# Optimization experiments

Measured on AMD Instinct MI355X. Metric: run time of the kernel, lower is better.

Reference implementation:

```python
import jax, jax.numpy as jnp
import numpy as np

B, S, T = 32, 512, 512           # batch, text len, decoder steps
ENC, ATT = 512, 128              # encoder_dim, attention_dim
PH, PO = 256, 256                # prenet hidden/output
DEC, M = 1024, 128               # decoder_rnn_dim, num_mels


def setup_inputs() -> dict:
    key = jax.random.key(0)
    ks = jax.random.split(key, 16)

    def w(k, shape, fan_in):
        return jax.random.normal(k, shape, jnp.float32) / np.float32(np.sqrt(fan_in))

    return {
        "encoder_outputs": jax.random.normal(ks[0], (B, S, ENC), jnp.float32),
        "target_mels": jax.random.normal(ks[1], (B, T, M), jnp.float32),
        # PreNet (dropout in eval mode => identity)
        "pn_w1": w(ks[2], (M, PH), M), "pn_b1": jnp.zeros((PH,), jnp.float32),
        "pn_w2": w(ks[3], (PH, PO), PH), "pn_b2": jnp.zeros((PO,), jnp.float32),
        # AdditiveAttention
        "att_we": w(ks[4], (ENC, ATT), ENC), "att_be": jnp.zeros((ATT,), jnp.float32),
        "att_wd": w(ks[5], (DEC, ATT), DEC), "att_bd": jnp.zeros((ATT,), jnp.float32),
        "att_v": w(ks[6], (ATT,), ATT), "att_vb": jnp.zeros((), jnp.float32),
        # GRU (PyTorch layout: W_ih [3H, in], W_hh [3H, H], gate order r,z,n)
        "gru_wih": w(ks[7], (3 * DEC, PO + ENC), PO + ENC),
        "gru_whh": w(ks[8], (3 * DEC, DEC), DEC),
        "gru_bih": jnp.zeros((3 * DEC,), jnp.float32),
        "gru_bhh": jnp.zeros((3 * DEC,), jnp.float32),
        # output / stop projections
        "out_w": w(ks[9], (DEC + ENC, M), DEC + ENC), "out_b": jnp.zeros((M,), jnp.float32),
        "stop_w": w(ks[10], (DEC + ENC, 1), DEC + ENC), "stop_b": jnp.zeros((1,), jnp.float32),
    }


def reference(encoder_outputs, target_mels, pn_w1, pn_b1, pn_w2, pn_b2,
              att_we, att_be, att_wd, att_bd, att_v, att_vb,
              gru_wih, gru_whh, gru_bih, gru_bhh,
              out_w, out_b, stop_w, stop_b):
    b, t, m = target_mels.shape
    # encoder projection is time-invariant: hoist out of the step loop
    enc_proj = encoder_outputs @ att_we + att_be              # [B,S,A]

    # teacher forcing: prev_mel at step 0 is zeros, then target_mels[:, t-1]
    prev_mels = jnp.concatenate(
        [jnp.zeros((1, b, m), target_mels.dtype),
         jnp.transpose(target_mels, (1, 0, 2))[:-1]], axis=0)  # [T,B,M]

    h0 = jnp.zeros((b, gru_whh.shape[1]), encoder_outputs.dtype)  # [B,DEC]

    def step(h, prev_mel):
        # PreNet (eval mode: dropout = identity)
        x = jax.nn.relu(prev_mel @ pn_w1 + pn_b1)
        x = jax.nn.relu(x @ pn_w2 + pn_b2)                     # [B,PO]
        # additive attention
        dproj = h @ att_wd + att_bd                            # [B,A]
        scores = jnp.tanh(enc_proj + dproj[:, None, :]) @ att_v + att_vb  # [B,S]
        aw = jax.nn.softmax(scores, axis=1)                    # [B,S]
        context = jnp.einsum('bs,bse->be', aw, encoder_outputs)  # [B,ENC]
        # GRU cell (PyTorch gate math, order r,z,n)
        rin = jnp.concatenate([x, context], axis=-1)           # [B,PO+ENC]
        gi = rin @ gru_wih.T + gru_bih                         # [B,3*DEC]
        gh = h @ gru_whh.T + gru_bhh
        ir, iz, inn = jnp.split(gi, 3, axis=-1)
        hr, hz, hn = jnp.split(gh, 3, axis=-1)
        r = jax.nn.sigmoid(ir + hr)
        z = jax.nn.sigmoid(iz + hz)
        n = jnp.tanh(inn + r * hn)
        h_new = (1.0 - z) * n + z * h                          # [B,DEC]
        # projections
        dout = jnp.concatenate([h_new, context], axis=-1)      # [B,DEC+ENC]
        mel = dout @ out_w + out_b                             # [B,M]
        stop = (dout @ stop_w + stop_b)[:, 0]                  # [B]
        return h_new, (mel, stop, aw)

    _, (mels, stops, aws) = jax.lax.scan(step, h0, prev_mels)
    mel_outputs = jnp.transpose(mels, (1, 0, 2))               # [B,T,M]
    stop_tokens = stops.T                                      # [B,T]
    attention_weights = jnp.transpose(aws, (1, 0, 2))          # [B,T,S]
    return (mel_outputs, stop_tokens, attention_weights)
```

## Files before the change

kernel.cpp:

```cpp
#include <hip/hip_runtime.h>

constexpr int B_   = 32;
constexpr int S_   = 512;
constexpr int T_   = 512;
constexpr int ENC_ = 512;
constexpr int ATT_ = 128;
constexpr int PO_  = 256;
constexpr int DEC_ = 1024;
constexpr int M_   = 128;

constexpr int MEL_OFF  = 0;
constexpr int STOP_OFF = B_*T_*M_;
constexpr int AW_OFF   = STOP_OFF + B_*T_;

typedef __attribute__((ext_vector_type(8))) short bf16x8;
typedef __attribute__((ext_vector_type(4))) float f32x4;
typedef unsigned long long ull;

__device__ __forceinline__ float frcp(float x){ return __builtin_amdgcn_rcpf(x); }
__device__ __forceinline__ float ftanh(float x){ float e = __expf(2.f*x); return 1.f - 2.f*frcp(e + 1.f); }
__device__ __forceinline__ float fsig(float x){ return frcp(1.f + __expf(-x)); }

__device__ __forceinline__ float2 upk2(unsigned u){
    return make_float2(__builtin_bit_cast(float, u << 16),
                       __builtin_bit_cast(float, u & 0xffff0000u));
}
__device__ __forceinline__ unsigned short f2b(float f){
    unsigned u = __builtin_bit_cast(unsigned, f);
    return (unsigned short)((u + 0x7fffu + ((u >> 16) & 1u)) >> 16);
}
__device__ __forceinline__ unsigned pk2(float a, float b){
    return (unsigned)f2b(a) | ((unsigned)f2b(b) << 16);
}

__device__ __forceinline__ float ald(const float* p){
    return __hip_atomic_load(p, __ATOMIC_RELAXED, __HIP_MEMORY_SCOPE_AGENT);
}
__device__ __forceinline__ ull ald64(const void* p){
    return __hip_atomic_load((const ull*)p, __ATOMIC_RELAXED, __HIP_MEMORY_SCOPE_AGENT);
}
__device__ __forceinline__ unsigned aldu(const unsigned* p){
    return __hip_atomic_load(p, __ATOMIC_RELAXED, __HIP_MEMORY_SCOPE_AGENT);
}
__device__ __forceinline__ void astf(float* p, float v){
    __hip_atomic_store(p, v, __ATOMIC_RELAXED, __HIP_MEMORY_SCOPE_AGENT);
}
union F2U { float2 f; ull u; };
__device__ __forceinline__ void ast2f(float* p, float a, float b){
    F2U x; x.f = make_float2(a, b);
    __hip_atomic_store((ull*)p, x.u, __ATOMIC_RELAXED, __HIP_MEMORY_SCOPE_AGENT);
}
__device__ __forceinline__ void astu(unsigned* p, unsigned v){
    __hip_atomic_store(p, v, __ATOMIC_RELAXED, __HIP_MEMORY_SCOPE_AGENT);
}

__device__ __forceinline__ void gbarF(unsigned* flags, unsigned ep){
    asm volatile("s_waitcnt vmcnt(0) lgkmcnt(0)" ::: "memory");
    __syncthreads();
    if (threadIdx.x == 0) astu(&flags[blockIdx.x*16], ep);
    if (threadIdx.x < 64){
        for (;;){
            unsigned m = 0xffffffffu;
            #pragma unroll
            for (int q = 0; q < 4; ++q){
                unsigned f = aldu(&flags[(threadIdx.x*4 + q)*16]);
                m = f < m ? f : m;
            }
            if (__all(m >= ep)) break;
            __builtin_amdgcn_s_sleep(1);
        }
    }
    __syncthreads();
}

__device__ __forceinline__ f32x4 mfma16(bf16x8 a, bf16x8 b, f32x4 c){
    return __builtin_amdgcn_mfma_f32_16x16x32_bf16(a, b, c, 0, 0, 0);
}

__global__ __launch_bounds__(256) void k_prep_w(const float* __restrict__ enc,
        const float* __restrict__ whh, const float* __restrict__ wih,
        const float* __restrict__ oww,
        unsigned short* __restrict__ enc_b, unsigned short* __restrict__ wgh,
        unsigned short* __restrict__ wgx, unsigned short* __restrict__ wgc,
        unsigned short* __restrict__ ow_b){
    long long idx = (long long)blockIdx.x*256 + threadIdx.x;
    if (idx < 8388608LL){
        int bh = (int)(idx >> 17); int r = (int)(idx & 131071);
        int s = r >> 9, e = r & 511;
        int b = bh >> 1, half = bh & 1;
        enc_b[idx] = f2b(enc[((size_t)b*S_ + half*256 + s)*ENC_ + e]);
    } else if (idx < 11534336LL){
        long long q = idx - 8388608LL;
        int ds = (int)(q / 98304); int r = (int)(q % 98304);
        int jc = r / 16384; int r2 = r % 16384;
        int kc = r2 >> 9, l = (r2 >> 3) & 63, e = r2 & 7;
        int j = (jc >> 1)*1024 + ds*32 + (jc & 1)*16 + (l & 15);
        int k = kc*32 + ((l >> 4) << 3) + e;
        wgh[q] = f2b(whh[(size_t)j*DEC_ + k]);
    } else if (idx < 12320768LL){
        long long q = idx - 11534336LL;
        int ds = (int)(q / 24576); int r = (int)(q % 24576);
        int jc = r / 4096; int r3 = r % 4096;
        int kc = r3 >> 9, l = (r3 >> 3) & 63, e = r3 & 7;
        int j = (jc >> 1)*1024 + ds*32 + (jc & 1)*16 + (l & 15);
        int k = kc*32 + ((l >> 4) << 3) + e;
        wgx[q] = f2b(wih[(size_t)j*768 + k]);
    } else if (idx < 13893632LL){
        long long q = idx - 12320768LL;
        int ds = (int)(q / 49152); int r = (int)(q % 49152);
        int jc = r / 8192; int r3 = r % 8192;
        int kc = r3 >> 9, l = (r3 >> 3) & 63, e = r3 & 7;
        int j = (jc >> 1)*1024 + ds*32 + (jc & 1)*16 + (l & 15);
        int k = kc*32 + ((l >> 4) << 3) + e;
        wgc[q] = f2b(wih[(size_t)j*768 + 256 + k]);
    } else if (idx < 14090240LL){
        long long q = idx - 13893632LL;
        int cg = (int)(q / 49152); int r = (int)(q % 49152);
        int oc = r / 1536, k = r % 1536;
        ow_b[q] = f2b(oww[(size_t)k*M_ + cg*32 + oc]);
    }
}

__global__ __launch_bounds__(256) void k_encproj(const float* __restrict__ enc,
        const float* __restrict__ we, const float* __restrict__ be,
        unsigned short* __restrict__ ep_b){
    __shared__ float we_s[64*128];
    __shared__ float enc_s[64*64];
    int blk = blockIdx.x, tid = threadIdx.x;
    int b = blk >> 3, ss = blk & 7;
    int s = tid >> 2, ag = tid & 3;
    float acc[32];
    #pragma unroll
    for (int j = 0; j < 32; ++j) acc[j] = 0.f;
    for (int kc = 0; kc < 8; ++kc){
        __syncthreads();
        for (int i = tid; i < 8192; i += 256)
            we_s[i] = we[(size_t)(kc*64 + (i >> 7))*ATT_ + (i & 127)];
        for (int i = tid; i < 4096; i += 256)
            enc_s[i] = enc[((size_t)b*S_ + ss*64 + (i >> 6))*ENC_ + kc*64 + (i & 63)];
        __syncthreads();
        for (int kk = 0; kk < 64; ++kk){
            float ev = enc_s[s*64 + kk];
            const float* wr = &we_s[(kk << 7) + (ag << 5)];
            #pragma unroll
            for (int j = 0; j < 32; ++j) acc[j] += ev*wr[j];
        }
    }
    #pragma unroll
    for (int j = 0; j < 32; ++j){
        int a = (ag << 5) + j;
        ep_b[((size_t)b*512 + ss*64 + s)*ATT_ + a] = f2b(acc[j] + be[a]);
    }
}

__global__ __launch_bounds__(128) void k_prenet(const float* __restrict__ tm,
        const float* __restrict__ w1, const float* __restrict__ b1,
        const float* __restrict__ w2, const float* __restrict__ b2,
        unsigned short* __restrict__ xall){
    __shared__ float mel_l[128*20];
    __shared__ float h1_l[256*20];
    int row0 = blockIdx.x << 4;
    int t = row0 >> 5, b0 = row0 & 31;
    int tid = threadIdx.x;
    for (int p = 0; p < 16; p++){
        int idx = tid + (p << 7);
        int k = idx & 127, r = idx >> 7;
        float v = 0.f;
        if (t > 0) v = tm[((size_t)(b0 + r)*T_ + (t - 1))*M_ + k];
        mel_l[k*20 + r] = v;
    }
    __syncthreads();
    float acc1[16], acc2[16];
    #pragma unroll
    for (int i = 0; i < 16; i++){ acc1[i] = 0.f; acc2[i] = 0.f; }
    for (int k = 0; k < M_; k++){
        float wa = w1[k*256 + tid];
        float wb = w1[k*256 + tid + 128];
        float mv[16];
        *(float4*)&mv[0]  = *(const float4*)&mel_l[k*20 + 0];
        *(float4*)&mv[4]  = *(const float4*)&mel_l[k*20 + 4];
        *(float4*)&mv[8]  = *(const float4*)&mel_l[k*20 + 8];
        *(float4*)&mv[12] = *(const float4*)&mel_l[k*20 + 12];
        #pragma unroll
        for (int r = 0; r < 16; r++){ acc1[r] += mv[r]*wa; acc2[r] += mv[r]*wb; }
    }
    float bb1a = b1[tid], bb1b = b1[tid + 128];
    #pragma unroll
    for (int r = 0; r < 16; r++){
        h1_l[tid*20 + r]         = fmaxf(acc1[r] + bb1a, 0.f);
        h1_l[(tid + 128)*20 + r] = fmaxf(acc2[r] + bb1b, 0.f);
    }
    __syncthreads();
    #pragma unroll
    for (int i = 0; i < 16; i++){ acc1[i] = 0.f; acc2[i] = 0.f; }
    for (int k = 0; k < 256; k++){
        float wa = w2[k*256 + tid];
        float wb = w2[k*256 + tid + 128];
        float mv[16];
        *(float4*)&mv[0]  = *(const float4*)&h1_l[k*20 + 0];
        *(float4*)&mv[4]  = *(const float4*)&h1_l[k*20 + 4];
        *(float4*)&mv[8]  = *(const float4*)&h1_l[k*20 + 8];
        *(float4*)&mv[12] = *(const float4*)&h1_l[k*20 + 12];
        #pragma unroll
        for (int r = 0; r < 16; r++){ acc1[r] += mv[r]*wa; acc2[r] += mv[r]*wb; }
    }
    float bb2a = b2[tid], bb2b = b2[tid + 128];
    #pragma unroll
    for (int r = 0; r < 16; r++){
        xall[((size_t)row0 + r)*PO_ + tid]       = f2b(fmaxf(acc1[r] + bb2a, 0.f));
        xall[((size_t)row0 + r)*PO_ + tid + 128] = f2b(fmaxf(acc2[r] + bb2b, 0.f));
    }
}

#define DYN_BYTES 110592

struct KP {
    const unsigned short* xall_b; const unsigned short* enc_b; const unsigned short* ep_b;
    const unsigned short* wgh; const unsigned short* wgx; const unsigned short* wgc;
    const unsigned short* ow_b;
    const float* awd; const float* sw; const float* bd; const float* av; const float* avb;
    const float* bih; const float* bhh; const float* p_ob; const float* p_sb;
    float* h_f32; unsigned short* h_fb;
    unsigned short* ctx_b; float* den; float* es_b; float* dpp;
    unsigned* flags; float* out;
};

__global__ __launch_bounds__(1024) void k_persist(KP p){
    extern __shared__ char sm[];
    const int bid = blockIdx.x, tid = threadIdx.x;
    const int lane = tid & 63;
    unsigned epn = 0;
    unsigned* flags = p.flags;

    if (bid < 64){
        const int xcd = bid & 7, slot8 = bid >> 3;
        const int ds = xcd*4 + (slot8 >> 1), bh = slot8 & 1;
        unsigned short* hf_b = (unsigned short*)sm;
        char* cf = sm;
        float* pgh_l = (float*)(sm + 32768);
        float* pgx_l = (float*)(sm + 45568);
        float* pgc_l = (float*)(sm + 58368);
        float* h_l   = (float*)(sm + 71168);
        float* rden_l= (float*)(sm + 73216);
        float h_reg = 0.f;

        for (int t = 0; t <= T_; ++t){
            if (t < T_){
                const ull* shb = (const ull*)p.h_fb;
                for (int i = tid; i < 4096; i += 1024){
                    int u = i & 1, l = (i >> 1) & 63, kc = i >> 7;
                    ((ull*)hf_b)[i] = ald64(&shb[(((size_t)bh*32 + kc)*64 + l)*2 + u]);
                }
                __syncthreads();
                int w = tid >> 6;
                if (w < 12){
                    int jc = w >> 1, kg = w & 1;
                    int r4 = lane >> 4, c16 = lane & 15;
                    const bf16x8* Bh = (const bf16x8*)p.wgh +
                        ((size_t)(ds*6 + jc)*32)*64 + lane;
                    f32x4 acc = {0.f,0.f,0.f,0.f};
                    #pragma unroll
                    for (int c = 0; c < 16; ++c){
                        int kc = kg*16 + c;
                        bf16x8 a = *(const bf16x8*)(hf_b + ((kc*64 + lane) << 3));
                        acc = mfma16(a, Bh[kc*64], acc);
                    }
                    #pragma unroll
                    for (int r = 0; r < 4; ++r)
                        pgh_l[(kg*16 + r4*4 + r)*100 + jc*16 + c16] = acc[r];
                    const bf16x8* Xp = (const bf16x8*)p.wgx +
                        ((size_t)(ds*6 + jc)*8)*64 + lane;
                    f32x4 ax = {0.f,0.f,0.f,0.f};
                    #pragma unroll
                    for (int c = 0; c < 4; ++c){
                        int kc = kg*4 + c;
                        bf16x8 a = *(const bf16x8*)(p.xall_b +
                            ((size_t)t*32 + bh*16 + c16)*256 + kc*32 + r4*8);
                        ax = mfma16(a, Xp[kc*64], ax);
                    }
                    #pragma unroll
                    for (int r = 0; r < 4; ++r)
                        pgx_l[(kg*16 + r4*4 + r)*100 + jc*16 + c16] = ax[r];
                }
            }
            gbarF(flags, ++epn);
            if (t < T_){
                const int slot = t & 1;
                if (tid < 16){
                    int b = bh*16 + tid;
                    rden_l[tid] = frcp(ald(&p.den[slot*64 + b]) +
                                       ald(&p.den[slot*64 + 32 + b]));
                }
                __syncthreads();
                {
                    int i = tid;
                    int kc = i >> 6, l = i & 63;
                    int b = bh*16 + (l & 15);
                    int e0 = kc*32 + ((l >> 4) << 3);
                    const ull* c0 = (const ull*)p.ctx_b + (((size_t)slot*2 + 0)*32 + b)*128 + (e0 >> 2);
                    const ull* c1 = (const ull*)p.ctx_b + (((size_t)slot*2 + 1)*32 + b)*128 + (e0 >> 2);
                    ull u00 = ald64(c0), u01 = ald64(c0 + 1);
                    ull u10 = ald64(c1), u11 = ald64(c1 + 1);
                    float rd = rden_l[l & 15];
                    uint2 x0 = __builtin_bit_cast(uint2, u00);
                    uint2 x1 = __builtin_bit_cast(uint2, u01);
                    uint2 y0 = __builtin_bit_cast(uint2, u10);
                    uint2 y1 = __builtin_bit_cast(uint2, u11);
                    float2 a0 = upk2(x0.x), b0 = upk2(y0.x);
                    float2 a1 = upk2(x0.y), b1 = upk2(y0.y);
                    float2 a2 = upk2(x1.x), b2 = upk2(y1.x);
                    float2 a3 = upk2(x1.y), b3 = upk2(y1.y);
                    unsigned w0 = pk2((a0.x + b0.x)*rd, (a0.y + b0.y)*rd);
                    unsigned w1 = pk2((a1.x + b1.x)*rd, (a1.y + b1.y)*rd);
                    unsigned w2 = pk2((a2.x + b2.x)*rd, (a2.y + b2.y)*rd);
                    unsigned w3 = pk2((a3.x + b3.x)*rd, (a3.y + b3.y)*rd);
                    *(uint4*)(cf + (size_t)i*16) = make_uint4(w0, w1, w2, w3);
                }
                __syncthreads();
                int w = tid >> 6;
                if (w < 12){
                    int jc = w >> 1, kg = w & 1;
                    int r4 = lane >> 4, c16 = lane & 15;
                    const bf16x8* Cp = (const bf16x8*)p.wgc +
                        ((size_t)(ds*6 + jc)*16)*64 + lane;
                    f32x4 acc = {0.f,0.f,0.f,0.f};
                    #pragma unroll
                    for (int c = 0; c < 8; ++c){
                        int kc = kg*8 + c;
                        bf16x8 a = *(const bf16x8*)(cf + ((kc*64 + lane) << 4));
                        acc = mfma16(a, Cp[kc*64], acc);
                    }
                    #pragma unroll
                    for (int r = 0; r < 4; ++r)
                        pgc_l[(kg*16 + r4*4 + r)*100 + jc*16 + c16] = acc[r];
                }
                __syncthreads();
                if (tid < 512){
                    int b16 = tid >> 5, dl = tid & 31;
                    int dglob = ds*32 + dl;
                    const float* pa = pgh_l + b16*100;
                    const float* pb = pgh_l + (16 + b16)*100;
                    const float* xa = pgx_l + b16*100;
                    const float* xb = pgx_l + (16 + b16)*100;
                    const float* ca = pgc_l + b16*100;
                    const float* cb = pgc_l + (16 + b16)*100;
                    float gi_r = xa[dl]      + xb[dl]      + ca[dl]      + cb[dl]      + p.bih[dglob];
                    float gi_z = xa[32 + dl] + xb[32 + dl] + ca[32 + dl] + cb[32 + dl] + p.bih[1024 + dglob];
                    float gi_n = xa[64 + dl] + xb[64 + dl] + ca[64 + dl] + cb[64 + dl] + p.bih[2048 + dglob];
                    float gh_r = pa[dl]      + pb[dl]      + p.bhh[dglob];
                    float gh_z = pa[32 + dl] + pb[32 + dl] + p.bhh[1024 + dglob];
                    float gh_n = pa[64 + dl] + pb[64 + dl] + p.bhh[2048 + dglob];
                    float rr = fsig(gi_r + gh_r);
                    float zz = fsig(gi_z + gh_z);
                    float nn = ftanh(gi_n + rr*gh_n);
                    float hv = (1.f - zz)*nn + zz*h_reg;
                    h_reg = hv;
                    h_l[b16*32 + dl] = hv;
                    float hv1 = __shfl_xor(hv, 1);
                    if (!(dl & 1)){
                        int b = bh*16 + b16;
                        ast2f(&p.h_f32[(size_t)((t + 1) & 1)*32768 + (size_t)b*1024 + dglob], hv, hv1);
                        unsigned pkv = pk2(hv, hv1);
                        int l2 = ((dl >> 3) << 4) + b16;
                        size_t fo = (((size_t)bh*32 + ds)*64 + l2)*4 + ((dl & 7) >> 1);
                        astu((unsigned*)p.h_fb + fo, pkv);
                    }
                }
                __syncthreads();
                {
                    int b16 = tid >> 6, ag = tid & 63;
                    int a0 = ag*2;
                    const float* ar = p.awd + (size_t)(ds*32)*128 + a0;
                    float s0 = 0.f, s1 = 0.f;
                    #pragma unroll 8
                    for (int dl = 0; dl < 32; ++dl){
                        float hd = h_l[b16*32 + dl];
                        float2 w2 = *(const float2*)(ar + (size_t)dl*128);
                        s0 += hd*w2.x; s1 += hd*w2.y;
                    }
                    ast2f(&p.dpp[(((size_t)ds*2 + bh)*16 + b16)*128 + a0], s0, s1);
                }
            }
            gbarF(flags, ++epn);
        }
    } else if (bid < 128){
        const int aa = bid - 64, b = aa >> 1, half = aa & 1;
        unsigned short* ep_l = (unsigned short*)sm;
        float* red  = (float*)(sm + 67584);
        float* sred = (float*)(sm + 100992);
        float* dpl  = (float*)(sm + 105088);
        float* avl  = (float*)(sm + 105600);
        float* esl  = (float*)(sm + 106112);
        float* eslt = (float*)(sm + 107136);
        {
            const ull* src = (const ull*)(p.ep_b + ((size_t)b*512 + half*256)*128);
            for (int i = tid; i < 8192; i += 1024){
                int row = i >> 5, col = i & 31;
                ((ull*)ep_l)[(size_t)row*33 + col] = src[i];
            }
            if (tid < 128) avl[tid] = p.av[tid];
        }
        __syncthreads();
        for (int t = 0; t <= T_; ++t){
            if (t < T_){
                const int slot = t & 1;
                {
                    int a = tid & 127, g = tid >> 7;
                    const int bhb = b >> 4, b15 = b & 15;
                    float s = 0.f;
                    #pragma unroll
                    for (int i = 0; i < 4; ++i){
                        int ds2 = g*4 + i;
                        s += ald(&p.dpp[(((size_t)ds2*2 + bhb)*16 + b15)*128 + a]);
                    }
                    red[g*128 + a] = s;
                }
                __syncthreads();
                if (tid < 128){
                    float s = p.bd[tid];
                    #pragma unroll
                    for (int g = 0; g < 8; ++g) s += red[g*128 + tid];
                    dpl[tid] = s;
                }
                __syncthreads();
                {
                    int s = tid >> 2, ao = tid & 3;
                    const ull* er = (const ull*)ep_l + (size_t)s*33 + ao*8;
                    float sc = 0.f;
                    #pragma unroll
                    for (int i = 0; i < 8; ++i){
                        uint2 uu = __builtin_bit_cast(uint2, er[i]);
                        float2 e0 = upk2(uu.x), e1 = upk2(uu.y);
                        int a0 = ao*32 + i*4;
                        sc += ftanh(e0.x + dpl[a0])*avl[a0]
                            + ftanh(e0.y + dpl[a0+1])*avl[a0+1]
                            + ftanh(e1.x + dpl[a0+2])*avl[a0+2]
                            + ftanh(e1.y + dpl[a0+3])*avl[a0+3];
                    }
                    sred[tid] = sc;
                }
                __syncthreads();
                if (tid < 256){
                    float sc = sred[tid*4] + sred[tid*4+1] + sred[tid*4+2] + sred[tid*4+3] + p.avb[0];
                    float ev = __expf(sc);
                    esl[tid] = ev;
                    eslt[(tid & 15)*17 + (tid >> 4)] = ev;
                    astf(&p.es_b[(size_t)slot*16384 + b*512 + half*256 + tid], ev);
                }
                __syncthreads();
                if (tid < 64){
                    float d = esl[tid*4] + esl[tid*4+1] + esl[tid*4+2] + esl[tid*4+3];
                    #pragma unroll
                    for (int m = 1; m <= 32; m <<= 1) d += __shfl_xor(d, m);
                    if (tid == 0) astf(&p.den[slot*64 + half*32 + b], d);
                }
                {
                    int eo = tid >> 4, sg = tid & 15;
                    int e8 = eo*8;
                    const unsigned short* eb = p.enc_b + ((size_t)b*2 + half)*131072;
                    float a0=0,a1=0,a2=0,a3=0,a4=0,a5=0,a6=0,a7=0;
                    #pragma unroll 4
                    for (int i = 0; i < 16; ++i){
                        int s = sg*16 + i;
                        float ev = eslt[i*17 + sg];
                        uint4 u = *(const uint4*)(eb + (size_t)s*512 + e8);
                        float2 v0=upk2(u.x), v1=upk2(u.y), v2=upk2(u.z), v3=upk2(u.w);
                        a0+=ev*v0.x; a1+=ev*v0.y; a2+=ev*v1.x; a3+=ev*v1.y;
                        a4+=ev*v2.x; a5+=ev*v2.y; a6+=ev*v3.x; a7+=ev*v3.y;
                    }
                    float* rr = &red[sg*522 + e8];
                    rr[0]=a0; rr[1]=a1; rr[2]=a2; rr[3]=a3;
                    rr[4]=a4; rr[5]=a5; rr[6]=a6; rr[7]=a7;
                }
                __syncthreads();
                if (tid < 512){
                    float c = 0.f;
                    #pragma unroll
                    for (int sg = 0; sg < 16; ++sg) c += red[sg*522 + tid];
                    float c1 = __shfl_xor(c, 1);
                    if (!(tid & 1))
                        astu((unsigned*)p.ctx_b + (((size_t)slot*2 + half)*32 + b)*256 + (tid >> 1),
                             pk2(c, c1));
                }
            }
            gbarF(flags, ++epn);
            gbarF(flags, ++epn);
        }
    } else {
        const int m = bid - 128, b = m >> 2, q = m & 3;
        unsigned short* ow_l = (unsigned short*)sm;
        float* dout = (float*)(sm + 98432);
        float* redm = (float*)(sm + 104576);
        float* rdm  = (float*)(sm + 108800);
        float* stpr = (float*)(sm + 108816);
        {
            const ull* src = (const ull*)p.ow_b + (size_t)q*12288;
            for (int i = tid; i < 12288; i += 1024){
                int oc = i / 384, kq = i - oc*384;
                uint2 u = __builtin_bit_cast(uint2, src[i]);
                unsigned* d = (unsigned*)ow_l + (size_t)oc*769 + kq*2;
                d[0] = u.x; d[1] = u.y;
            }
        }
        __syncthreads();
        for (int t = 0; t <= T_; ++t){
            gbarF(flags, ++epn);
            if (t >= 1){
                const int slot = (t - 1) & 1;
                if (tid < 512){
                    ull u = ald64((const ull*)p.h_f32 + (size_t)(t & 1)*16384 + (size_t)b*512 + tid);
                    *(float2*)&dout[tid*2] = __builtin_bit_cast(float2, u);
                } else if (tid < 768){
                    int i = tid - 512;
                    unsigned u0 = aldu((const unsigned*)p.ctx_b + (((size_t)slot*2 + 0)*32 + b)*256 + i);
                    unsigned u1 = aldu((const unsigned*)p.ctx_b + (((size_t)slot*2 + 1)*32 + b)*256 + i);
                    float2 f0 = upk2(u0), f1 = upk2(u1);
                    *(float2*)&dout[1024 + i*2] = make_float2(f0.x + f1.x, f0.y + f1.y);
                } else if (tid == 1023){
                    rdm[0] = frcp(ald(&p.den[slot*64 + b]) + ald(&p.den[slot*64 + 32 + b]));
                }
                __syncthreads();
                if (tid < 512) dout[1024 + tid] *= rdm[0];
                __syncthreads();
                {
                    int kg = tid >> 5, oc = tid & 31;
                    const unsigned* wr = (const unsigned*)ow_l + (size_t)oc*769 + kg*24;
                    const float* dr = dout + kg*48;
                    float a = 0.f;
                    #pragma unroll 6
                    for (int i = 0; i < 24; ++i){
                        float2 w2 = upk2(wr[i]);
                        a += dr[i*2]*w2.x + dr[i*2+1]*w2.y;
                    }
                    redm[kg*33 + oc] = a;
                }
                if (q == 0 && tid < 512){
                    int k3 = tid*3;
                    float s = dout[k3]*p.sw[k3] + dout[k3+1]*p.sw[k3+1] + dout[k3+2]*p.sw[k3+2];
                    #pragma unroll
                    for (int mm = 1; mm <= 32; mm <<= 1) s += __shfl_xor(s, mm);
                    if ((tid & 63) == 0) stpr[tid >> 6] = s;
                    float ev = ald(&p.es_b[(size_t)slot*16384 + b*512 + tid]);
                    p.out[AW_OFF + ((size_t)b*T_ + (t-1))*S_ + tid] = ev*rdm[0];
                }
                __syncthreads();
                if (tid < 32){
                    float a = 0.f;
                    #pragma unroll
                    for (int kg = 0; kg < 32; ++kg) a += redm[kg*33 + tid];
                    int c = q*32 + tid;
                    p.out[MEL_OFF + ((size_t)b*T_ + (t-1))*M_ + c] = a + p.p_ob[c];
                } else if (tid == 32 && q == 0){
                    float tot = 0.f;
                    #pragma unroll
                    for (int w2 = 0; w2 < 8; ++w2) tot += stpr[w2];
                    p.out[STOP_OFF + (size_t)b*T_ + (t-1)] = tot + p.p_sb[0];
                }
            }
            gbarF(flags, ++epn);
        }
    }
}

extern "C" void kernel_launch(void* const* d_in, const int* in_sizes, int n_in,
                              void* d_out, int out_size, void* d_ws, size_t ws_size,
                              hipStream_t stream){
    const float* enc = (const float*)d_in[0];
    const float* tm  = (const float*)d_in[1];
    const float* pw1 = (const float*)d_in[2];
    const float* pb1 = (const float*)d_in[3];
    const float* pw2 = (const float*)d_in[4];
    const float* pb2 = (const float*)d_in[5];
    const float* awe = (const float*)d_in[6];
    const float* abe = (const float*)d_in[7];
    const float* awd = (const float*)d_in[8];
    const float* abd = (const float*)d_in[9];
    const float* av  = (const float*)d_in[10];
    const float* avb = (const float*)d_in[11];
    const float* wih = (const float*)d_in[12];
    const float* whh = (const float*)d_in[13];
    const float* bih = (const float*)d_in[14];
    const float* bhh = (const float*)d_in[15];
    const float* oww = (const float*)d_in[16];
    const float* obb = (const float*)d_in[17];
    const float* sww = (const float*)d_in[18];
    const float* sbb = (const float*)d_in[19];
    float* out = (float*)d_out;
    float* ws  = (float*)d_ws;

    unsigned short* xall_b = (unsigned short*)ws;
    unsigned short* enc_b  = (unsigned short*)(ws + 2097152);
    unsigned short* ep_b   = (unsigned short*)(ws + 6291456);
    unsigned short* wgh    = (unsigned short*)(ws + 7340032);
    unsigned short* wgx    = (unsigned short*)(ws + 8912896);
    unsigned short* wgc    = (unsigned short*)(ws + 9306112);
    unsigned short* ow_b   = (unsigned short*)(ws + 10092544);
    float* h_f32 = ws + 10190848;
    unsigned short* h_fb   = (unsigned short*)(ws + 10256384);
    unsigned short* ctx_b  = (unsigned short*)(ws + 10272768);
    float* den  = ws + 10305536;
    float* es_b = ws + 10305664;
    float* dpp  = ws + 10338432;
    unsigned* flags = (unsigned*)(ws + 10469504);

    hipMemsetAsync(h_f32, 0, (size_t)65536*4, stream);
    hipMemsetAsync(h_fb, 0, 32768*2, stream);
    hipMemsetAsync(dpp, 0, (size_t)131072*4, stream);
    hipMemsetAsync(flags, 0, 16384, stream);

    k_prep_w<<<55040, 256, 0, stream>>>(enc, whh, wih, oww,
                                        enc_b, wgh, wgx, wgc, ow_b);
    k_encproj<<<256, 256, 0, stream>>>(enc, awe, abe, ep_b);
    k_prenet<<<1024, 128, 0, stream>>>(tm, pw1, pb1, pw2, pb2, xall_b);

    hipFuncSetAttribute((const void*)k_persist,
                        hipFuncAttributeMaxDynamicSharedMemorySize, DYN_BYTES);

    KP kp;
    kp.xall_b = xall_b; kp.enc_b = enc_b; kp.ep_b = ep_b;
    kp.wgh = wgh; kp.wgx = wgx; kp.wgc = wgc; kp.ow_b = ow_b;
    kp.awd = awd; kp.sw = sww; kp.bd = abd; kp.av = av; kp.avb = avb;
    kp.bih = bih; kp.bhh = bhh; kp.p_ob = obb; kp.p_sb = sbb;
    kp.h_f32 = h_f32; kp.h_fb = h_fb;
    kp.ctx_b = ctx_b; kp.den = den; kp.es_b = es_b; kp.dpp = dpp;
    kp.flags = flags; kp.out = out;

    KP* kparg = &kp;
    void* args[] = { (void*)kparg };
    hipLaunchCooperativeKernel((void*)k_persist, dim3(256), dim3(1024),
                               args, DYN_BYTES, stream);
}
```

Before: 15.68 ms.

## Replace global barriers with per-role producer-consumer flags and deeper buffering

Replaces the two all-block grid barriers per step with per-role flags (GRU, attention, output blocks), so each role waits only on the producers it actually reads. Buffers for h, context, den and scores are deepened (h to double or quad slots, context and scores to 4 slots), which lets the output-projection blocks lag behind the recurrence by up to a few steps. The aim is to take the output projection and other waits off the critical path of the sequential GRU/attention loop. In exchange it adds more flag polling, more workspace, and tricky slot-reuse correctness.

```diff
diff --git a/kernel.cpp b/kernel.cpp
--- a/kernel.cpp
+++ b/kernel.cpp
@@ -54,23 +54,32 @@
     __hip_atomic_store(p, v, __ATOMIC_RELAXED, __HIP_MEMORY_SCOPE_AGENT);
 }
 
-__device__ __forceinline__ void gbarF(unsigned* flags, unsigned ep){
+__device__ __forceinline__ void waitP64(const unsigned* f, unsigned ep){
+    if (threadIdx.x < 64){
+        for (;;){
+            unsigned v = aldu(&f[threadIdx.x*16]);
+            if (__all(v >= ep)) break;
+            __builtin_amdgcn_s_sleep(1);
+        }
+    }
+    __syncthreads();
+}
+__device__ __forceinline__ void waitP128(const unsigned* f, unsigned ep){
+    if (threadIdx.x < 64){
+        for (;;){
+            unsigned a = aldu(&f[threadIdx.x*16]);
+            unsigned b = aldu(&f[(threadIdx.x + 64)*16]);
+            unsigned m = a < b ? a : b;
+            if (__all(m >= ep)) break;
+            __builtin_amdgcn_s_sleep(1);
+        }
+    }
+    __syncthreads();
+}
+__device__ __forceinline__ void signalF(unsigned* f, unsigned v){
     asm volatile("s_waitcnt vmcnt(0) lgkmcnt(0)" ::: "memory");
     __syncthreads();
-    if (threadIdx.x == 0) astu(&flags[blockIdx.x*16], ep);
-    if (threadIdx.x < 64){
-        for (;;){
-            unsigned m = 0xffffffffu;
-            #pragma unroll
-            for (int q = 0; q < 4; ++q){
-                unsigned f = aldu(&flags[(threadIdx.x*4 + q)*16]);
-                m = f < m ? f : m;
-            }
-            if (__all(m >= ep)) break;
-            __builtin_amdgcn_s_sleep(1);
-        }
-    }
-    __syncthreads();
+    if (threadIdx.x == 0) astu(f, v);
 }
 
 __device__ __forceinline__ f32x4 mfma16(bf16x8 a, bf16x8 b, f32x4 c){
@@ -222,15 +231,13 @@
     const float* bih; const float* bhh; const float* p_ob; const float* p_sb;
     float* h_f32; unsigned short* h_fb;
     unsigned short* ctx_b; float* den; float* es_b; float* dpp;
-    unsigned* flags; float* out;
+    unsigned* gflag; unsigned* aflag; unsigned* mflag; float* out;
 };
 
 __global__ __launch_bounds__(1024) void k_persist(KP p){
     extern __shared__ char sm[];
     const int bid = blockIdx.x, tid = threadIdx.x;
     const int lane = tid & 63;
-    unsigned epn = 0;
-    unsigned* flags = p.flags;
 
     if (bid < 64){
         const int xcd = bid & 7, slot8 = bid >> 3;
@@ -244,9 +251,10 @@
         float* rden_l= (float*)(sm + 73216);
         float h_reg = 0.f;
 
-        for (int t = 0; t <= T_; ++t){
-            if (t < T_){
-                const ull* shb = (const ull*)p.h_fb;
+        for (int t = 0; t < T_; ++t){
+            waitP64(p.gflag, (unsigned)t);
+            {
+                const ull* shb = (const ull*)p.h_fb + (size_t)(t & 1)*8192;
                 for (int i = tid; i < 4096; i += 1024){
                     int u = i & 1, l = (i >> 1) & 63, kc = i >> 7;
                     ((ull*)hf_b)[i] = ald64(&shb[(((size_t)bh*32 + kc)*64 + l)*2 + u]);
@@ -282,10 +290,11 @@
                     for (int r = 0; r < 4; ++r)
                         pgx_l[(kg*16 + r4*4 + r)*100 + jc*16 + c16] = ax[r];
                 }
-            }
-            gbarF(flags, ++epn);
-            if (t < T_){
-                const int slot = t & 1;
+                __syncthreads();
+            }
+            waitP64(p.aflag, (unsigned)(t + 1));
+            {
+                const int slot = t & 3;
                 if (tid < 16){
                     int b = bh*16 + tid;
                     rden_l[tid] = frcp(ald(&p.den[slot*64 + b]) +
@@ -359,10 +368,11 @@
                     float hv1 = __shfl_xor(hv, 1);
                     if (!(dl & 1)){
                         int b = bh*16 + b16;
-                        ast2f(&p.h_f32[(size_t)((t + 1) & 1)*32768 + (size_t)b*1024 + dglob], hv, hv1);
+                        ast2f(&p.h_f32[(size_t)((t + 1) & 3)*32768 + (size_t)b*1024 + dglob], hv, hv1);
                         unsigned pkv = pk2(hv, hv1);
                         int l2 = ((dl >> 3) << 4) + b16;
-                        size_t fo = (((size_t)bh*32 + ds)*64 + l2)*4 + ((dl & 7) >> 1);
+                        size_t fo = (size_t)((t + 1) & 1)*16384 +
+                                    (((size_t)bh*32 + ds)*64 + l2)*4 + ((dl & 7) >> 1);
                         astu((unsigned*)p.h_fb + fo, pkv);
                     }
                 }
@@ -381,7 +391,7 @@
                     ast2f(&p.dpp[(((size_t)ds*2 + bh)*16 + b16)*128 + a0], s0, s1);
                 }
             }
-            gbarF(flags, ++epn);
+            signalF(&p.gflag[bid*16], (unsigned)(t + 1));
         }
     } else if (bid < 128){
         const int aa = bid - 64, b = aa >> 1, half = aa & 1;
@@ -401,90 +411,89 @@
             if (tid < 128) avl[tid] = p.av[tid];
         }
         __syncthreads();
-        for (int t = 0; t <= T_; ++t){
-            if (t < T_){
-                const int slot = t & 1;
-                {
-                    int a = tid & 127, g = tid >> 7;
-                    const int bhb = b >> 4, b15 = b & 15;
-                    float s = 0.f;
-                    #pragma unroll
-                    for (int i = 0; i < 4; ++i){
-                        int ds2 = g*4 + i;
-                        s += ald(&p.dpp[(((size_t)ds2*2 + bhb)*16 + b15)*128 + a]);
-                    }
-                    red[g*128 + a] = s;
-                }
-                __syncthreads();
-                if (tid < 128){
-                    float s = p.bd[tid];
-                    #pragma unroll
-                    for (int g = 0; g < 8; ++g) s += red[g*128 + tid];
-                    dpl[tid] = s;
-                }
-                __syncthreads();
-                {
-                    int s = tid >> 2, ao = tid & 3;
-                    const ull* er = (const ull*)ep_l + (size_t)s*33 + ao*8;
-                    float sc = 0.f;
-                    #pragma unroll
-                    for (int i = 0; i < 8; ++i){
-                        uint2 uu = __builtin_bit_cast(uint2, er[i]);
-                        float2 e0 = upk2(uu.x), e1 = upk2(uu.y);
-                        int a0 = ao*32 + i*4;
-                        sc += ftanh(e0.x + dpl[a0])*avl[a0]
-                            + ftanh(e0.y + dpl[a0+1])*avl[a0+1]
-                            + ftanh(e1.x + dpl[a0+2])*avl[a0+2]
-                            + ftanh(e1.y + dpl[a0+3])*avl[a0+3];
-                    }
-                    sred[tid] = sc;
-                }
-                __syncthreads();
-                if (tid < 256){
-                    float sc = sred[tid*4] + sred[tid*4+1] + sred[tid*4+2] + sred[tid*4+3] + p.avb[0];
-                    float ev = __expf(sc);
-                    esl[tid] = ev;
-                    eslt[(tid & 15)*17 + (tid >> 4)] = ev;
-                    astf(&p.es_b[(size_t)slot*16384 + b*512 + half*256 + tid], ev);
-                }
-                __syncthreads();
-                if (tid < 64){
-                    float d = esl[tid*4] + esl[tid*4+1] + esl[tid*4+2] + esl[tid*4+3];
-                    #pragma unroll
-                    for (int m = 1; m <= 32; m <<= 1) d += __shfl_xor(d, m);
-                    if (tid == 0) astf(&p.den[slot*64 + half*32 + b], d);
-                }
-                {
-                    int eo = tid >> 4, sg = tid & 15;
-                    int e8 = eo*8;
-                    const unsigned short* eb = p.enc_b + ((size_t)b*2 + half)*131072;
-                    float a0=0,a1=0,a2=0,a3=0,a4=0,a5=0,a6=0,a7=0;
-                    #pragma unroll 4
-                    for (int i = 0; i < 16; ++i){
-                        int s = sg*16 + i;
-                        float ev = eslt[i*17 + sg];
-                        uint4 u = *(const uint4*)(eb + (size_t)s*512 + e8);
-                        float2 v0=upk2(u.x), v1=upk2(u.y), v2=upk2(u.z), v3=upk2(u.w);
-                        a0+=ev*v0.x; a1+=ev*v0.y; a2+=ev*v1.x; a3+=ev*v1.y;
-                        a4+=ev*v2.x; a5+=ev*v2.y; a6+=ev*v3.x; a7+=ev*v3.y;
-                    }
-                    float* rr = &red[sg*522 + e8];
-                    rr[0]=a0; rr[1]=a1; rr[2]=a2; rr[3]=a3;
-                    rr[4]=a4; rr[5]=a5; rr[6]=a6; rr[7]=a7;
-                }
-                __syncthreads();
-                if (tid < 512){
-                    float c = 0.f;
-                    #pragma unroll
-                    for (int sg = 0; sg < 16; ++sg) c += red[sg*522 + tid];
-                    float c1 = __shfl_xor(c, 1);
-                    if (!(tid & 1))
-                        astu((unsigned*)p.ctx_b + (((size_t)slot*2 + half)*32 + b)*256 + (tid >> 1),
-                             pk2(c, c1));
-                }
-            }
-            gbarF(flags, ++epn);
-            gbarF(flags, ++epn);
+        for (int t = 0; t < T_; ++t){
+            waitP64(p.gflag, (unsigned)t);
+            if (t >= 3) waitP128(p.mflag, (unsigned)(t - 2));
+            const int slot = t & 3;
+            {
+                int a = tid & 127, g = tid >> 7;
+                const int bhb = b >> 4, b15 = b & 15;
+                float s = 0.f;
+                #pragma unroll
+                for (int i = 0; i < 4; ++i){
+                    int ds2 = g*4 + i;
+                    s += ald(&p.dpp[(((size_t)ds2*2 + bhb)*16 + b15)*128 + a]);
+                }
+                red[g*128 + a] = s;
+            }
+            __syncthreads();
+            if (tid < 128){
+                float s = p.bd[tid];
+                #pragma unroll
+                for (int g = 0; g < 8; ++g) s += red[g*128 + tid];
+                dpl[tid] = s;
+            }
+            __syncthreads();
+            {
+                int s = tid >> 2, ao = tid & 3;
+                const ull* er = (const ull*)ep_l + (size_t)s*33 + ao*8;
+                float sc = 0.f;
+                #pragma unroll
+                for (int i = 0; i < 8; ++i){
+                    uint2 uu = __builtin_bit_cast(uint2, er[i]);
+                    float2 e0 = upk2(uu.x), e1 = upk2(uu.y);
+                    int a0 = ao*32 + i*4;
+                    sc += ftanh(e0.x + dpl[a0])*avl[a0]
+                        + ftanh(e0.y + dpl[a0+1])*avl[a0+1]
+                        + ftanh(e1.x + dpl[a0+2])*avl[a0+2]
+                        + ftanh(e1.y + dpl[a0+3])*avl[a0+3];
+                }
+                sred[tid] = sc;
+            }
+            __syncthreads();
+            if (tid < 256){
+                float sc = sred[tid*4] + sred[tid*4+1] + sred[tid*4+2] + sred[tid*4+3] + p.avb[0];
+                float ev = __expf(sc);
+                esl[tid] = ev;
+                eslt[(tid & 15)*17 + (tid >> 4)] = ev;
+                astf(&p.es_b[(size_t)slot*16384 + b*512 + half*256 + tid], ev);
+            }
+            __syncthreads();
+            if (tid < 64){
+                float d = esl[tid*4] + esl[tid*4+1] + esl[tid*4+2] + esl[tid*4+3];
+                #pragma unroll
+                for (int m = 1; m <= 32; m <<= 1) d += __shfl_xor(d, m);
+                if (tid == 0) astf(&p.den[slot*64 + half*32 + b], d);
+            }
+            {
+                int eo = tid >> 4, sg = tid & 15;
+                int e8 = eo*8;
+                const unsigned short* eb = p.enc_b + ((size_t)b*2 + half)*131072;
+                float a0=0,a1=0,a2=0,a3=0,a4=0,a5=0,a6=0,a7=0;
+                #pragma unroll 4
+                for (int i = 0; i < 16; ++i){
+                    int s = sg*16 + i;
+                    float ev = eslt[i*17 + sg];
+                    uint4 u = *(const uint4*)(eb + (size_t)s*512 + e8);
+                    float2 v0=upk2(u.x), v1=upk2(u.y), v2=upk2(u.z), v3=upk2(u.w);
+                    a0+=ev*v0.x; a1+=ev*v0.y; a2+=ev*v1.x; a3+=ev*v1.y;
+                    a4+=ev*v2.x; a5+=ev*v2.y; a6+=ev*v3.x; a7+=ev*v3.y;
+                }
+                float* rr = &red[sg*522 + e8];
+                rr[0]=a0; rr[1]=a1; rr[2]=a2; rr[3]=a3;
+                rr[4]=a4; rr[5]=a5; rr[6]=a6; rr[7]=a7;
+            }
+            __syncthreads();
+            if (tid < 512){
+                float c = 0.f;
+                #pragma unroll
+                for (int sg = 0; sg < 16; ++sg) c += red[sg*522 + tid];
+                float c1 = __shfl_xor(c, 1);
+                if (!(tid & 1))
+                    astu((unsigned*)p.ctx_b + (((size_t)slot*2 + half)*32 + b)*256 + (tid >> 1),
+                         pk2(c, c1));
+            }
+            signalF(&p.aflag[aa*16], (unsigned)(t + 1));
         }
     } else {
         const int m = bid - 128, b = m >> 2, q = m & 3;
@@ -503,61 +512,60 @@
             }
         }
         __syncthreads();
-        for (int t = 0; t <= T_; ++t){
-            gbarF(flags, ++epn);
-            if (t >= 1){
-                const int slot = (t - 1) & 1;
-                if (tid < 512){
-                    ull u = ald64((const ull*)p.h_f32 + (size_t)(t & 1)*16384 + (size_t)b*512 + tid);
-                    *(float2*)&dout[tid*2] = __builtin_bit_cast(float2, u);
-                } else if (tid < 768){
-                    int i = tid - 512;
-                    unsigned u0 = aldu((const unsigned*)p.ctx_b + (((size_t)slot*2 + 0)*32 + b)*256 + i);
-                    unsigned u1 = aldu((const unsigned*)p.ctx_b + (((size_t)slot*2 + 1)*32 + b)*256 + i);
-                    float2 f0 = upk2(u0), f1 = upk2(u1);
-                    *(float2*)&dout[1024 + i*2] = make_float2(f0.x + f1.x, f0.y + f1.y);
-                } else if (tid == 1023){
-                    rdm[0] = frcp(ald(&p.den[slot*64 + b]) + ald(&p.den[slot*64 + 32 + b]));
-                }
-                __syncthreads();
-                if (tid < 512) dout[1024 + tid] *= rdm[0];
-                __syncthreads();
-                {
-                    int kg = tid >> 5, oc = tid & 31;
-                    const unsigned* wr = (const unsigned*)ow_l + (size_t)oc*769 + kg*24;
-                    const float* dr = dout + kg*48;
-                    float a = 0.f;
-                    #pragma unroll 6
-                    for (int i = 0; i < 24; ++i){
-                        float2 w2 = upk2(wr[i]);
-                        a += dr[i*2]*w2.x + dr[i*2+1]*w2.y;
-                    }
-                    redm[kg*33 + oc] = a;
-                }
-                if (q == 0 && tid < 512){
-                    int k3 = tid*3;
-                    float s = dout[k3]*p.sw[k3] + dout[k3+1]*p.sw[k3+1] + dout[k3+2]*p.sw[k3+2];
-                    #pragma unroll
-                    for (int mm = 1; mm <= 32; mm <<= 1) s += __shfl_xor(s, mm);
-                    if ((tid & 63) == 0) stpr[tid >> 6] = s;
-                    float ev = ald(&p.es_b[(size_t)slot*16384 + b*512 + tid]);
-                    p.out[AW_OFF + ((size_t)b*T_ + (t-1))*S_ + tid] = ev*rdm[0];
-                }
-                __syncthreads();
-                if (tid < 32){
-                    float a = 0.f;
-                    #pragma unroll
-                    for (int kg = 0; kg < 32; ++kg) a += redm[kg*33 + tid];
-                    int c = q*32 + tid;
-                    p.out[MEL_OFF + ((size_t)b*T_ + (t-1))*M_ + c] = a + p.p_ob[c];
-                } else if (tid == 32 && q == 0){
-                    float tot = 0.f;
-                    #pragma unroll
-                    for (int w2 = 0; w2 < 8; ++w2) tot += stpr[w2];
-                    p.out[STOP_OFF + (size_t)b*T_ + (t-1)] = tot + p.p_sb[0];
-                }
-            }
-            gbarF(flags, ++epn);
+        for (int t = 1; t <= T_; ++t){
+            waitP64(p.gflag, (unsigned)t);
+            waitP64(p.aflag, (unsigned)t);
+            const int slot = (t - 1) & 3;
+            if (tid < 512){
+                ull u = ald64((const ull*)p.h_f32 + (size_t)(t & 3)*16384 + (size_t)b*512 + tid);
+                *(float2*)&dout[tid*2] = __builtin_bit_cast(float2, u);
+            } else if (tid < 768){
+                int i = tid - 512;
+                unsigned u0 = aldu((const unsigned*)p.ctx_b + (((size_t)slot*2 + 0)*32 + b)*256 + i);
+                unsigned u1 = aldu((const unsigned*)p.ctx_b + (((size_t)slot*2 + 1)*32 + b)*256 + i);
+                float2 f0 = upk2(u0), f1 = upk2(u1);
+                *(float2*)&dout[1024 + i*2] = make_float2(f0.x + f1.x, f0.y + f1.y);
+            } else if (tid == 1023){
+                rdm[0] = frcp(ald(&p.den[slot*64 + b]) + ald(&p.den[slot*64 + 32 + b]));
+            }
+            __syncthreads();
+            if (tid < 512) dout[1024 + tid] *= rdm[0];
+            __syncthreads();
+            {
+                int kg = tid >> 5, oc = tid & 31;
+                const unsigned* wr = (const unsigned*)ow_l + (size_t)oc*769 + kg*24;
+                const float* dr = dout + kg*48;
+                float a = 0.f;
+                #pragma unroll 6
+                for (int i = 0; i < 24; ++i){
+                    float2 w2 = upk2(wr[i]);
+                    a += dr[i*2]*w2.x + dr[i*2+1]*w2.y;
+                }
+                redm[kg*33 + oc] = a;
+            }
+            if (q == 0 && tid < 512){
+                int k3 = tid*3;
+                float s = dout[k3]*p.sw[k3] + dout[k3+1]*p.sw[k3+1] + dout[k3+2]*p.sw[k3+2];
+                #pragma unroll
+                for (int mm = 1; mm <= 32; mm <<= 1) s += __shfl_xor(s, mm);
+                if ((tid & 63) == 0) stpr[tid >> 6] = s;
+                float ev = ald(&p.es_b[(size_t)slot*16384 + b*512 + tid]);
+                p.out[AW_OFF + ((size_t)b*T_ + (t-1))*S_ + tid] = ev*rdm[0];
+            }
+            __syncthreads();
+            if (tid < 32){
+                float a = 0.f;
+                #pragma unroll
+                for (int kg = 0; kg < 32; ++kg) a += redm[kg*33 + tid];
+                int c = q*32 + tid;
+                p.out[MEL_OFF + ((size_t)b*T_ + (t-1))*M_ + c] = a + p.p_ob[c];
+            } else if (tid == 32 && q == 0){
+                float tot = 0.f;
+                #pragma unroll
+                for (int w2 = 0; w2 < 8; ++w2) tot += stpr[w2];
+                p.out[STOP_OFF + (size_t)b*T_ + (t-1)] = tot + p.p_sb[0];
+            }
+            signalF(&p.mflag[m*16], (unsigned)t);
         }
     }
 }
@@ -596,17 +604,19 @@
     unsigned short* wgc    = (unsigned short*)(ws + 9306112);
     unsigned short* ow_b   = (unsigned short*)(ws + 10092544);
     float* h_f32 = ws + 10190848;
-    unsigned short* h_fb   = (unsigned short*)(ws + 10256384);
-    unsigned short* ctx_b  = (unsigned short*)(ws + 10272768);
-    float* den  = ws + 10305536;
-    float* es_b = ws + 10305664;
-    float* dpp  = ws + 10338432;
-    unsigned* flags = (unsigned*)(ws + 10469504);
-
-    hipMemsetAsync(h_f32, 0, (size_t)65536*4, stream);
-    hipMemsetAsync(h_fb, 0, 32768*2, stream);
+    unsigned short* h_fb   = (unsigned short*)(ws + 10321920);
+    unsigned short* ctx_b  = (unsigned short*)(ws + 10354688);
+    float* den  = ws + 10420224;
+    float* es_b = ws + 10420480;
+    float* dpp  = ws + 10486016;
+    unsigned* gflag = (unsigned*)(ws + 10617088);
+    unsigned* aflag = gflag + 1024;
+    unsigned* mflag = aflag + 1024;
+
+    hipMemsetAsync(h_f32, 0, (size_t)131072*4, stream);
+    hipMemsetAsync(h_fb, 0, (size_t)65536*2, stream);
     hipMemsetAsync(dpp, 0, (size_t)131072*4, stream);
-    hipMemsetAsync(flags, 0, 16384, stream);
+    hipMemsetAsync(gflag, 0, 16384, stream);
 
     k_prep_w<<<55040, 256, 0, stream>>>(enc, whh, wih, oww,
                                         enc_b, wgh, wgx, wgc, ow_b);
@@ -623,7 +633,7 @@
     kp.bih = bih; kp.bhh = bhh; kp.p_ob = obb; kp.p_sb = sbb;
     kp.h_f32 = h_f32; kp.h_fb = h_fb;
     kp.ctx_b = ctx_b; kp.den = den; kp.es_b = es_b; kp.dpp = dpp;
-    kp.flags = flags; kp.out = out;
+    kp.gflag = gflag; kp.aflag = aflag; kp.mflag = mflag; kp.out = out;
 
     KP* kparg = &kp;
     void* args[] = { (void*)kparg };
```

Result: faster. 15.28 ms (-2.5%).
